# Performance work log

Measured on AMD Instinct MI355X. Metric: run time of the kernel, lower is better.

Reference implementation:

```python
import jax, jax.numpy as jnp
import numpy as np

INPUT_DIM = 1024
NUM_HEADS = 16
HEAD_DIM = INPUT_DIM // NUM_HEADS


def setup_inputs() -> dict:
    key = jax.random.key(0)
    ks = jax.random.split(key, 9)
    d = INPUT_DIM
    s = 1.0 / np.sqrt(d)
    x = jax.random.normal(ks[0], (2, 2048, d), dtype=jnp.float32)
    # nn.Linear default init ~ U(-1/sqrt(in), 1/sqrt(in)); weights stored as (out, in), we keep (in, out)
    Wq = jax.random.uniform(ks[1], (d, d), jnp.float32, -s, s)
    bq = jax.random.uniform(ks[2], (d,), jnp.float32, -s, s)
    Wk = jax.random.uniform(ks[3], (d, d), jnp.float32, -s, s)
    bk = jax.random.uniform(ks[4], (d,), jnp.float32, -s, s)
    Wv = jax.random.uniform(ks[5], (d, d), jnp.float32, -s, s)
    bv = jax.random.uniform(ks[6], (d,), jnp.float32, -s, s)
    Wo = jax.random.uniform(ks[7], (d, d), jnp.float32, -s, s)
    bo = jax.random.uniform(ks[8], (d,), jnp.float32, -s, s)
    return {"x": x, "Wq": Wq, "bq": bq, "Wk": Wk, "bk": bk, "Wv": Wv, "bv": bv, "Wo": Wo, "bo": bo}


def reference(x, Wq, bq, Wk, bk, Wv, bv, Wo, bo):
    b, t, d = x.shape
    h, hd = NUM_HEADS, HEAD_DIM
    # projections -> [b, h, t, hd]
    q = (x @ Wq + bq).reshape(b, t, h, hd).transpose(0, 2, 1, 3)
    k = (x @ Wk + bk).reshape(b, t, h, hd).transpose(0, 2, 1, 3)
    v = (x @ Wv + bv).reshape(b, t, h, hd).transpose(0, 2, 1, 3)
    scores = jnp.einsum('bhqd,bhkd->bhqk', q, k) / jnp.sqrt(jnp.float32(hd))
    probs = jax.nn.softmax(scores, axis=-1)
    out = jnp.einsum('bhqk,bhkd->bhqd', probs, v)
    out = out.transpose(0, 2, 1, 3).reshape(b, t, d)
    return out @ Wo + bo
```

## Files before the change

kernel.cpp:

```cpp
#include <hip/hip_runtime.h>
#include <math.h>


#define BATCH 2
#define SEQ   2048
#define DIM   1024
#define NHEAD 16
#define HDIM  64
#define MROWS (BATCH * SEQ)
#define BH    (BATCH * NHEAD)

typedef __attribute__((ext_vector_type(4))) float     floatx4;
typedef __attribute__((ext_vector_type(4))) float     float4v;
typedef __attribute__((ext_vector_type(8))) _Float16  half8;
typedef __attribute__((ext_vector_type(4))) _Float16  half4;
typedef __attribute__((ext_vector_type(2))) __fp16    fp16x2;

#define SOFT_C 5.77078016f
#define QSCALE 0.18033688f

#if __has_builtin(__builtin_amdgcn_exp2f)
#define EXP2F(x) __builtin_amdgcn_exp2f(x)
#else
#define EXP2F(x) exp2f(x)
#endif

__device__ __forceinline__ void gload16(const void* g, void* l) {
    __builtin_amdgcn_global_load_lds(
        (const __attribute__((address_space(1))) unsigned int*)g,
        (__attribute__((address_space(3))) unsigned int*)l, 16, 0, 0);
}

__device__ __forceinline__ unsigned pk2(float a, float b) {
    fp16x2 v = __builtin_amdgcn_cvt_pkrtz(a, b);
    return __builtin_bit_cast(unsigned, v);
}

__global__ __launch_bounds__(256) void prep(
    const float* __restrict__ x,
    const float* __restrict__ Wq, const float* __restrict__ Wk,
    const float* __restrict__ Wv, const float* __restrict__ Wo,
    _Float16* __restrict__ xh,
    _Float16* __restrict__ Wqt, _Float16* __restrict__ Wkt,
    _Float16* __restrict__ Wvt, _Float16* __restrict__ Wot)
{
    const int tid = threadIdx.x;
    if (blockIdx.z == 4) {
        const int bid = blockIdx.y * 16 + blockIdx.x;
        #pragma unroll
        for (int it = 0; it < 8; ++it) {
            const size_t i = (((size_t)it * 256 + bid) * 256 + tid) * 8;
            float4v a = *(const float4v*)(x + i);
            float4v b = *(const float4v*)(x + i + 4);
            half8 o;
            #pragma unroll
            for (int c = 0; c < 4; ++c) { o[c] = (_Float16)a[c]; o[4+c] = (_Float16)b[c]; }
            *(half8*)(xh + i) = o;
        }
        return;
    }
    __shared__ float tile[64][65];
    const float* W; _Float16* o;
    switch (blockIdx.z) {
        case 0: W = Wq; o = Wqt; break;
        case 1: W = Wk; o = Wkt; break;
        case 2: W = Wv; o = Wvt; break;
        default: W = Wo; o = Wot; break;
    }
    const int n0 = blockIdx.x * 64, k0 = blockIdx.y * 64;
    #pragma unroll
    for (int p = 0; p < 16; ++p) {
        int idx = tid + p * 256;
        int r = idx >> 6, c = idx & 63;
        tile[r][c] = W[(size_t)(k0 + r) * DIM + n0 + c];
    }
    __syncthreads();
    #pragma unroll
    for (int p = 0; p < 16; ++p) {
        int idx = tid + p * 256;
        int r = idx >> 6, c = idx & 63;
        o[(size_t)(n0 + r) * DIM + k0 + c] = (_Float16)tile[c][r];
    }
}

__device__ __forceinline__ void gemm_core16(
    const _Float16* __restrict__ Ap, const _Float16* __restrict__ Bp,
    int m0, int n0, _Float16* AL, _Float16* BL, floatx4 acc[4][4])
{
    const int tid  = threadIdx.x;
    const int wave = tid >> 6;
    const int lane = tid & 63;
    const int li   = lane & 15;
    const int quad = lane >> 4;
    const int wm   = (wave >> 1) * 64;
    const int wn   = (wave & 1) * 64;

    for (int kt = 0; kt < DIM / 64; ++kt) {
        __syncthreads();
        const int k0 = kt * 64;
        #pragma unroll
        for (int p = 0; p < 4; ++p) {
            int s = tid + p * 256;
            int r = s >> 3, ks = s & 7;
            int kg = (ks ^ (r & 7)) << 3;
            int ldsb = (wave * 64 + p * 256) * 8;
            gload16(Ap + (size_t)(m0 + r) * DIM + k0 + kg, AL + ldsb);
            gload16(Bp + (size_t)(n0 + r) * DIM + k0 + kg, BL + ldsb);
        }
        __syncthreads();

        half8 a[4][2], b[4][2];
        #pragma unroll
        for (int i = 0; i < 4; ++i) {
            int ra = (wm + i * 16 + li) << 6;
            int rb = (wn + i * 16 + li) << 6;
            #pragma unroll
            for (int h = 0; h < 2; ++h) {
                a[i][h] = *(const half8*)(AL + ra + (((h * 4 + quad) ^ (li & 7)) << 3));
                b[i][h] = *(const half8*)(BL + rb + (((h * 4 + quad) ^ (li & 7)) << 3));
            }
        }
        #pragma unroll
        for (int i = 0; i < 4; ++i)
            #pragma unroll
            for (int j = 0; j < 4; ++j) {
                acc[i][j] = __builtin_amdgcn_mfma_f32_16x16x32_f16(a[i][0], b[j][0], acc[i][j], 0, 0, 0);
                acc[i][j] = __builtin_amdgcn_mfma_f32_16x16x32_f16(a[i][1], b[j][1], acc[i][j], 0, 0, 0);
            }
    }
}

__global__ __launch_bounds__(256, 3) void qkv_mfma(
    const _Float16* __restrict__ xh,
    const _Float16* __restrict__ Wqt, const _Float16* __restrict__ Wkt,
    const _Float16* __restrict__ Wvt,
    const float* __restrict__ bq, const float* __restrict__ bk,
    const float* __restrict__ bv,
    _Float16* __restrict__ Qh, _Float16* __restrict__ Kh,
    _Float16* __restrict__ Vth)
{
    __shared__ __align__(16) _Float16 SH[128 * 136];
    _Float16* AL = SH;
    _Float16* BL = SH + 128 * 64;

    const int z = blockIdx.z;
    const _Float16* Bp; const float* bias;
    if (z == 0)      { Bp = Wqt; bias = bq; }
    else if (z == 1) { Bp = Wkt; bias = bk; }
    else             { Bp = Wvt; bias = bv; }

    const int m0 = blockIdx.y * 128, n0 = blockIdx.x * 128;

    floatx4 acc[4][4];
    #pragma unroll
    for (int i = 0; i < 4; ++i)
        #pragma unroll
        for (int j = 0; j < 4; ++j) acc[i][j] = (floatx4){0.f, 0.f, 0.f, 0.f};

    gemm_core16(xh, Bp, m0, n0, AL, BL, acc);

    const int tid = threadIdx.x, wave = tid >> 6, lane = tid & 63;
    const int li = lane & 15, quad = lane >> 4;
    const int wm = (wave >> 1) * 64, wn = (wave & 1) * 64;
    const int bb = m0 >> 11, t0 = m0 & 2047;

    if (z != 2) {
        _Float16* out = (z == 0) ? Qh : Kh;
        const float sc = (z == 0) ? QSCALE : 1.0f;
        #pragma unroll
        for (int i = 0; i < 4; ++i)
            #pragma unroll
            for (int j = 0; j < 4; ++j) {
                int n = n0 + wn + j * 16 + li;
                int h = n >> 6, hd = n & 63;
                float b_ = bias[n];
                #pragma unroll
                for (int r = 0; r < 4; ++r) {
                    int m = m0 + wm + i * 16 + quad * 4 + r;
                    int t = m & 2047;
                    out[(((size_t)(bb * NHEAD + h) * SEQ) + t) * HDIM + hd] =
                        (_Float16)((acc[i][j][r] + b_) * sc);
                }
            }
    } else {
        __syncthreads();
        #pragma unroll
        for (int i = 0; i < 4; ++i)
            #pragma unroll
            for (int j = 0; j < 4; ++j) {
                int n = wn + j * 16 + li;
                float b_ = bias[n0 + n];
                half4 w;
                #pragma unroll
                for (int r = 0; r < 4; ++r) w[r] = (_Float16)(acc[i][j][r] + b_);
                *(half4*)(SH + n * 136 + wm + i * 16 + quad * 4) = w;
            }
        __syncthreads();
        #pragma unroll
        for (int p = 0; p < 8; ++p) {
            int idx = p * 256 + tid;
            int v = idx >> 4, c8 = (idx & 15) * 8;
            half8 w = *(const half8*)(SH + v * 136 + c8);
            int n = n0 + v;
            int h = n >> 6, hd = n & 63;
            *(half8*)(Vth + ((size_t)(bb * NHEAD + h) * HDIM + hd) * SEQ + t0 + c8) = w;
        }
    }
}

#define LDP 72

__global__ __launch_bounds__(256) void attn(
    const _Float16* __restrict__ Q, const _Float16* __restrict__ K,
    const _Float16* __restrict__ Vt, _Float16* __restrict__ Ctx)
{
    __shared__ __align__(16) _Float16 Ks[64 * 64];
    __shared__ __align__(16) _Float16 Vs[64 * 64];
    __shared__ __align__(16) _Float16 Pt[4][32 * LDP];

    const int tid  = threadIdx.x;
    const int wave = tid >> 6;
    const int lane = tid & 63;
    const int li   = lane & 15;
    const int quad = lane >> 4;
    const int bh   = blockIdx.y;
    const int q0   = blockIdx.x * 128;
    const int b    = bh >> 4, h = bh & 15;

    half8 qa[2][2];
    #pragma unroll
    for (int nq = 0; nq < 2; ++nq) {
        size_t qrow = ((size_t)bh * SEQ + q0 + wave * 32 + nq * 16 + li) * HDIM;
        qa[nq][0] = *(const half8*)(Q + qrow + quad * 8);
        qa[nq][1] = *(const half8*)(Q + qrow + 32 + quad * 8);
    }

    half8 onesA;
    {
        _Float16 v = (li == 0) ? (_Float16)1.0f : (_Float16)0.0f;
        #pragma unroll
        for (int c = 0; c < 8; ++c) onesA[c] = v;
    }

    floatx4 O[4][2];
    floatx4 rsacc[2];
    #pragma unroll
    for (int nq = 0; nq < 2; ++nq) {
        rsacc[nq] = (floatx4){0.f, 0.f, 0.f, 0.f};
        #pragma unroll
        for (int i = 0; i < 4; ++i) O[i][nq] = (floatx4){0.f, 0.f, 0.f, 0.f};
    }

    const _Float16* Kbh = K  + (size_t)bh * SEQ * HDIM;
    const _Float16* Vbh = Vt + (size_t)bh * HDIM * SEQ;
    _Float16* Pw = Pt[wave];

    for (int kt = 0; kt < SEQ / 64; ++kt) {
        __syncthreads();
        {
            const _Float16* Kg = Kbh + (size_t)kt * 64 * HDIM;
            const _Float16* Vg = Vbh + kt * 64;
            #pragma unroll
            for (int p = 0; p < 2; ++p) {
                int s = tid + p * 256;
                int r = s >> 3, ks = s & 7;
                int kg = (ks ^ (r & 7)) << 3;
                int ldsb = (wave * 64 + p * 256) * 8;
                gload16(Kg + r * HDIM + kg, (_Float16*)Ks + ldsb);
                gload16(Vg + (size_t)r * SEQ + kg, (_Float16*)Vs + ldsb);
            }
        }
        __syncthreads();

        #pragma unroll
        for (int mb = 0; mb < 4; ++mb) {
            int row = (mb * 16 + li) << 6;
            half8 a0 = *(const half8*)(Ks + row + ((quad ^ (li & 7)) << 3));
            half8 a1 = *(const half8*)(Ks + row + (((quad + 4) ^ (li & 7)) << 3));
            #pragma unroll
            for (int nq = 0; nq < 2; ++nq) {
                floatx4 st = (floatx4){-SOFT_C, -SOFT_C, -SOFT_C, -SOFT_C};
                st = __builtin_amdgcn_mfma_f32_16x16x32_f16(a0, qa[nq][0], st, 0, 0, 0);
                st = __builtin_amdgcn_mfma_f32_16x16x32_f16(a1, qa[nq][1], st, 0, 0, 0);
                uint2 w;
                w.x = pk2(EXP2F(st[0]), EXP2F(st[1]));
                w.y = pk2(EXP2F(st[2]), EXP2F(st[3]));
                *(uint2*)(Pw + (nq * 16 + li) * LDP + mb * 16 + quad * 4) = w;
            }
        }

        half8 pb[2][2];
        #pragma unroll
        for (int nq = 0; nq < 2; ++nq) {
            pb[nq][0] = *(const half8*)(Pw + (nq * 16 + li) * LDP + quad * 8);
            pb[nq][1] = *(const half8*)(Pw + (nq * 16 + li) * LDP + 32 + quad * 8);
        }
        #pragma unroll
        for (int nq = 0; nq < 2; ++nq) {
            rsacc[nq] = __builtin_amdgcn_mfma_f32_16x16x32_f16(onesA, pb[nq][0], rsacc[nq], 0, 0, 0);
            rsacc[nq] = __builtin_amdgcn_mfma_f32_16x16x32_f16(onesA, pb[nq][1], rsacc[nq], 0, 0, 0);
        }
        #pragma unroll
        for (int mb = 0; mb < 4; ++mb) {
            int row = (mb * 16 + li) << 6;
            half8 v0 = *(const half8*)(Vs + row + ((quad ^ (li & 7)) << 3));
            half8 v1 = *(const half8*)(Vs + row + (((quad + 4) ^ (li & 7)) << 3));
            #pragma unroll
            for (int nq = 0; nq < 2; ++nq) {
                O[mb][nq] = __builtin_amdgcn_mfma_f32_16x16x32_f16(v0, pb[nq][0], O[mb][nq], 0, 0, 0);
                O[mb][nq] = __builtin_amdgcn_mfma_f32_16x16x32_f16(v1, pb[nq][1], O[mb][nq], 0, 0, 0);
            }
        }
    }

    float inv[2];
    #pragma unroll
    for (int nq = 0; nq < 2; ++nq) {
        float r = __shfl(rsacc[nq][0], li, 64);
        inv[nq] = 1.0f / r;
    }

    #pragma unroll
    for (int mb = 0; mb < 4; ++mb)
        #pragma unroll
        for (int nq = 0; nq < 2; ++nq) {
            uint2 w;
            w.x = pk2(O[mb][nq][0] * inv[nq], O[mb][nq][1] * inv[nq]);
            w.y = pk2(O[mb][nq][2] * inv[nq], O[mb][nq][3] * inv[nq]);
            *(uint2*)(Pw + (nq * 16 + li) * LDP + mb * 16 + quad * 4) = w;
        }
    #pragma unroll
    for (int p = 0; p < 4; ++p) {
        int idx = p * 64 + lane;
        int qq = idx >> 3, c8 = (idx & 7) * 8;
        half8 v = *(const half8*)(Pw + qq * LDP + c8);
        size_t row = (size_t)b * SEQ + q0 + wave * 32 + qq;
        *(half8*)(Ctx + row * DIM + h * HDIM + c8) = v;
    }
}

__global__ __launch_bounds__(256, 3) void out_mfma(
    const _Float16* __restrict__ Ctx, const _Float16* __restrict__ Wot,
    const float* __restrict__ bo, float* __restrict__ out)
{
    __shared__ __align__(16) _Float16 AL[128 * 64];
    __shared__ __align__(16) _Float16 BL[128 * 64];

    const int m0 = blockIdx.y * 128, n0 = blockIdx.x * 128;

    floatx4 acc[4][4];
    #pragma unroll
    for (int i = 0; i < 4; ++i)
        #pragma unroll
        for (int j = 0; j < 4; ++j) acc[i][j] = (floatx4){0.f, 0.f, 0.f, 0.f};

    gemm_core16(Ctx, Wot, m0, n0, AL, BL, acc);

    const int tid = threadIdx.x, wave = tid >> 6, lane = tid & 63;
    const int li = lane & 15, quad = lane >> 4;
    const int wm = (wave >> 1) * 64, wn = (wave & 1) * 64;

    #pragma unroll
    for (int i = 0; i < 4; ++i)
        #pragma unroll
        for (int j = 0; j < 4; ++j) {
            int n = n0 + wn + j * 16 + li;
            float b_ = bo[n];
            #pragma unroll
            for (int r = 0; r < 4; ++r) {
                int m = m0 + wm + i * 16 + quad * 4 + r;
                out[(size_t)m * DIM + n] = acc[i][j][r] + b_;
            }
        }
}

extern "C" void kernel_launch(void* const* d_in, const int* in_sizes, int n_in,
                              void* d_out, int out_size, void* d_ws, size_t ws_size,
                              hipStream_t stream) {
    const float* x  = (const float*)d_in[0];
    const float* Wq = (const float*)d_in[1];
    const float* bq = (const float*)d_in[2];
    const float* Wk = (const float*)d_in[3];
    const float* bk = (const float*)d_in[4];
    const float* Wv = (const float*)d_in[5];
    const float* bv = (const float*)d_in[6];
    const float* Wo = (const float*)d_in[7];
    const float* bo = (const float*)d_in[8];
    float* out = (float*)d_out;

    const size_t PX = (size_t)MROWS * DIM;
    const size_t PW = (size_t)DIM * DIM;
    _Float16* xh  = (_Float16*)d_ws;
    _Float16* Wqt = xh + PX;
    _Float16* Wkt = Wqt + PW;
    _Float16* Wvt = Wkt + PW;
    _Float16* Wot = Wvt + PW;
    _Float16* Qh  = Wot + PW;
    _Float16* Kh  = Qh + PX;
    _Float16* Vth = Kh + PX;

    _Float16* Ctx = xh;

    prep<<<dim3(16, 16, 5), 256, 0, stream>>>(
        x, Wq, Wk, Wv, Wo, xh, Wqt, Wkt, Wvt, Wot);

    qkv_mfma<<<dim3(DIM / 128, MROWS / 128, 3), 256, 0, stream>>>(
        xh, Wqt, Wkt, Wvt, bq, bk, bv, Qh, Kh, Vth);

    attn<<<dim3(SEQ / 128, BH), 256, 0, stream>>>(Qh, Kh, Vth, Ctx);

    out_mfma<<<dim3(DIM / 128, MROWS / 128), 256, 0, stream>>>(
        Ctx, Wot, bo, out);
}
```

Baseline: 201.2 us.

## Double-buffer K/V tiles in attention and relax GEMM launch bounds

The attention kernel now keeps two LDS buffers for the K and V tiles. It issues the global-to-LDS loads for the next key tile before computing on the current one, which hides load latency and removes one barrier per iteration. The cost is twice the LDS for K/V, which may lower attention occupancy. The QKV and output GEMM kernels also drop the minimum blocks-per-CU hint from 3 to 2, giving the compiler more register room at the cost of possible occupancy.

```diff
diff --git a/kernel.cpp b/kernel.cpp
--- a/kernel.cpp
+++ b/kernel.cpp
@@ -130,7 +130,7 @@
     }
 }
 
-__global__ __launch_bounds__(256, 3) void qkv_mfma(
+__global__ __launch_bounds__(256, 2) void qkv_mfma(
     const _Float16* __restrict__ xh,
     const _Float16* __restrict__ Wqt, const _Float16* __restrict__ Wkt,
     const _Float16* __restrict__ Wvt,
@@ -214,8 +214,8 @@
     const _Float16* __restrict__ Q, const _Float16* __restrict__ K,
     const _Float16* __restrict__ Vt, _Float16* __restrict__ Ctx)
 {
-    __shared__ __align__(16) _Float16 Ks[64 * 64];
-    __shared__ __align__(16) _Float16 Vs[64 * 64];
+    __shared__ __align__(16) _Float16 Ks[2][64 * 64];
+    __shared__ __align__(16) _Float16 Vs[2][64 * 64];
     __shared__ __align__(16) _Float16 Pt[4][32 * LDP];
 
     const int tid  = threadIdx.x;
@@ -255,28 +255,38 @@
     const _Float16* Vbh = Vt + (size_t)bh * HDIM * SEQ;
     _Float16* Pw = Pt[wave];
 
+    const int s0r = tid >> 3,           s0k = tid & 7;
+    const int s1r = (tid + 256) >> 3,   s1k = (tid + 256) & 7;
+    const int kg0 = (s0k ^ (s0r & 7)) << 3;
+    const int kg1 = (s1k ^ (s1r & 7)) << 3;
+    const int lb0 = (wave * 64) * 8;
+    const int lb1 = (wave * 64 + 256) * 8;
+
+    #define STAGE(buf, kt)                                                     \
+        do {                                                                   \
+            const _Float16* Kg = Kbh + (size_t)(kt) * 64 * HDIM;               \
+            const _Float16* Vg = Vbh + (kt) * 64;                              \
+            gload16(Kg + s0r * HDIM + kg0, Ks[buf] + lb0);                     \
+            gload16(Vg + (size_t)s0r * SEQ + kg0, Vs[buf] + lb0);              \
+            gload16(Kg + s1r * HDIM + kg1, Ks[buf] + lb1);                     \
+            gload16(Vg + (size_t)s1r * SEQ + kg1, Vs[buf] + lb1);              \
+        } while (0)
+
+    STAGE(0, 0);
+
     for (int kt = 0; kt < SEQ / 64; ++kt) {
+        const int cur = kt & 1;
         __syncthreads();
-        {
-            const _Float16* Kg = Kbh + (size_t)kt * 64 * HDIM;
-            const _Float16* Vg = Vbh + kt * 64;
-            #pragma unroll
-            for (int p = 0; p < 2; ++p) {
-                int s = tid + p * 256;
-                int r = s >> 3, ks = s & 7;
-                int kg = (ks ^ (r & 7)) << 3;
-                int ldsb = (wave * 64 + p * 256) * 8;
-                gload16(Kg + r * HDIM + kg, (_Float16*)Ks + ldsb);
-                gload16(Vg + (size_t)r * SEQ + kg, (_Float16*)Vs + ldsb);
-            }
-        }
-        __syncthreads();
+        if (kt + 1 < SEQ / 64) STAGE(cur ^ 1, kt + 1);
+
+        const _Float16* Kc = Ks[cur];
+        const _Float16* Vc = Vs[cur];
 
         #pragma unroll
         for (int mb = 0; mb < 4; ++mb) {
             int row = (mb * 16 + li) << 6;
-            half8 a0 = *(const half8*)(Ks + row + ((quad ^ (li & 7)) << 3));
-            half8 a1 = *(const half8*)(Ks + row + (((quad + 4) ^ (li & 7)) << 3));
+            half8 a0 = *(const half8*)(Kc + row + ((quad ^ (li & 7)) << 3));
+            half8 a1 = *(const half8*)(Kc + row + (((quad + 4) ^ (li & 7)) << 3));
             #pragma unroll
             for (int nq = 0; nq < 2; ++nq) {
                 floatx4 st = (floatx4){-SOFT_C, -SOFT_C, -SOFT_C, -SOFT_C};
@@ -303,8 +313,8 @@
         #pragma unroll
         for (int mb = 0; mb < 4; ++mb) {
             int row = (mb * 16 + li) << 6;
-            half8 v0 = *(const half8*)(Vs + row + ((quad ^ (li & 7)) << 3));
-            half8 v1 = *(const half8*)(Vs + row + (((quad + 4) ^ (li & 7)) << 3));
+            half8 v0 = *(const half8*)(Vc + row + ((quad ^ (li & 7)) << 3));
+            half8 v1 = *(const half8*)(Vc + row + (((quad + 4) ^ (li & 7)) << 3));
             #pragma unroll
             for (int nq = 0; nq < 2; ++nq) {
                 O[mb][nq] = __builtin_amdgcn_mfma_f32_16x16x32_f16(v0, pb[nq][0], O[mb][nq], 0, 0, 0);
@@ -312,6 +322,7 @@
             }
         }
     }
+    #undef STAGE
 
     float inv[2];
     #pragma unroll
@@ -339,7 +350,7 @@
     }
 }
 
-__global__ __launch_bounds__(256, 3) void out_mfma(
+__global__ __launch_bounds__(256, 2) void out_mfma(
     const _Float16* __restrict__ Ctx, const _Float16* __restrict__ Wot,
     const float* __restrict__ bo, float* __restrict__ out)
 {
```

Result: slower. 206.0 us (+2.4%).

## Load K/V fragments directly from global into registers with double buffering

Applied to the files above, without the earlier changes.

Drops the shared-memory staging of K and V tiles and the two block barriers per tile in the attention kernel. Each wave now loads its own K and V MFMA fragments straight from global memory into registers, double-buffered so the next tile's loads overlap the current tile's math. Because the tile is no longer shared, each of the four waves fetches the same K/V data separately, which quadruples global/L2 traffic and raises register pressure. The launch-bounds occupancy hints on all three kernels are also lowered from 3 to 2 to leave room for the extra registers.

```diff
diff --git a/kernel.cpp b/kernel.cpp
--- a/kernel.cpp
+++ b/kernel.cpp
@@ -130,7 +130,7 @@
     }
 }
 
-__global__ __launch_bounds__(256, 3) void qkv_mfma(
+__global__ __launch_bounds__(256, 2) void qkv_mfma(
     const _Float16* __restrict__ xh,
     const _Float16* __restrict__ Wqt, const _Float16* __restrict__ Wkt,
     const _Float16* __restrict__ Wvt,
@@ -210,12 +210,22 @@
 
 #define LDP 72
 
-__global__ __launch_bounds__(256) void attn(
+__device__ __forceinline__ void load_frag(
+    const _Float16* __restrict__ base, size_t rstride, int li, int quad,
+    half8 f[4][2])
+{
+    #pragma unroll
+    for (int mb = 0; mb < 4; ++mb) {
+        const _Float16* p = base + (size_t)(mb * 16 + li) * rstride + quad * 8;
+        f[mb][0] = *(const half8*)(p);
+        f[mb][1] = *(const half8*)(p + 32);
+    }
+}
+
+__global__ __launch_bounds__(256, 2) void attn(
     const _Float16* __restrict__ Q, const _Float16* __restrict__ K,
     const _Float16* __restrict__ Vt, _Float16* __restrict__ Ctx)
 {
-    __shared__ __align__(16) _Float16 Ks[64 * 64];
-    __shared__ __align__(16) _Float16 Vs[64 * 64];
     __shared__ __align__(16) _Float16 Pt[4][32 * LDP];
 
     const int tid  = threadIdx.x;
@@ -255,63 +265,58 @@
     const _Float16* Vbh = Vt + (size_t)bh * HDIM * SEQ;
     _Float16* Pw = Pt[wave];
 
-    for (int kt = 0; kt < SEQ / 64; ++kt) {
-        __syncthreads();
-        {
-            const _Float16* Kg = Kbh + (size_t)kt * 64 * HDIM;
-            const _Float16* Vg = Vbh + kt * 64;
-            #pragma unroll
-            for (int p = 0; p < 2; ++p) {
-                int s = tid + p * 256;
-                int r = s >> 3, ks = s & 7;
-                int kg = (ks ^ (r & 7)) << 3;
-                int ldsb = (wave * 64 + p * 256) * 8;
-                gload16(Kg + r * HDIM + kg, (_Float16*)Ks + ldsb);
-                gload16(Vg + (size_t)r * SEQ + kg, (_Float16*)Vs + ldsb);
-            }
-        }
-        __syncthreads();
-
-        #pragma unroll
-        for (int mb = 0; mb < 4; ++mb) {
-            int row = (mb * 16 + li) << 6;
-            half8 a0 = *(const half8*)(Ks + row + ((quad ^ (li & 7)) << 3));
-            half8 a1 = *(const half8*)(Ks + row + (((quad + 4) ^ (li & 7)) << 3));
-            #pragma unroll
-            for (int nq = 0; nq < 2; ++nq) {
-                floatx4 st = (floatx4){-SOFT_C, -SOFT_C, -SOFT_C, -SOFT_C};
-                st = __builtin_amdgcn_mfma_f32_16x16x32_f16(a0, qa[nq][0], st, 0, 0, 0);
-                st = __builtin_amdgcn_mfma_f32_16x16x32_f16(a1, qa[nq][1], st, 0, 0, 0);
-                uint2 w;
-                w.x = pk2(EXP2F(st[0]), EXP2F(st[1]));
-                w.y = pk2(EXP2F(st[2]), EXP2F(st[3]));
-                *(uint2*)(Pw + (nq * 16 + li) * LDP + mb * 16 + quad * 4) = w;
-            }
-        }
-
-        half8 pb[2][2];
-        #pragma unroll
-        for (int nq = 0; nq < 2; ++nq) {
-            pb[nq][0] = *(const half8*)(Pw + (nq * 16 + li) * LDP + quad * 8);
-            pb[nq][1] = *(const half8*)(Pw + (nq * 16 + li) * LDP + 32 + quad * 8);
-        }
-        #pragma unroll
-        for (int nq = 0; nq < 2; ++nq) {
-            rsacc[nq] = __builtin_amdgcn_mfma_f32_16x16x32_f16(onesA, pb[nq][0], rsacc[nq], 0, 0, 0);
-            rsacc[nq] = __builtin_amdgcn_mfma_f32_16x16x32_f16(onesA, pb[nq][1], rsacc[nq], 0, 0, 0);
-        }
-        #pragma unroll
-        for (int mb = 0; mb < 4; ++mb) {
-            int row = (mb * 16 + li) << 6;
-            half8 v0 = *(const half8*)(Vs + row + ((quad ^ (li & 7)) << 3));
-            half8 v1 = *(const half8*)(Vs + row + (((quad + 4) ^ (li & 7)) << 3));
-            #pragma unroll
-            for (int nq = 0; nq < 2; ++nq) {
-                O[mb][nq] = __builtin_amdgcn_mfma_f32_16x16x32_f16(v0, pb[nq][0], O[mb][nq], 0, 0, 0);
-                O[mb][nq] = __builtin_amdgcn_mfma_f32_16x16x32_f16(v1, pb[nq][1], O[mb][nq], 0, 0, 0);
-            }
-        }
-    }
+    #define ATTN_BODY(kf, vf)                                                  \
+        do {                                                                   \
+            _Pragma("unroll")                                                  \
+            for (int mb = 0; mb < 4; ++mb) {                                   \
+                _Pragma("unroll")                                              \
+                for (int nq = 0; nq < 2; ++nq) {                               \
+                    floatx4 st = (floatx4){-SOFT_C, -SOFT_C, -SOFT_C, -SOFT_C};\
+                    st = __builtin_amdgcn_mfma_f32_16x16x32_f16(kf[mb][0], qa[nq][0], st, 0, 0, 0); \
+                    st = __builtin_amdgcn_mfma_f32_16x16x32_f16(kf[mb][1], qa[nq][1], st, 0, 0, 0); \
+                    uint2 w;                                                   \
+                    w.x = pk2(EXP2F(st[0]), EXP2F(st[1]));                     \
+                    w.y = pk2(EXP2F(st[2]), EXP2F(st[3]));                     \
+                    *(uint2*)(Pw + (nq * 16 + li) * LDP + mb * 16 + quad * 4) = w; \
+                }                                                              \
+            }                                                                  \
+            half8 pb[2][2];                                                    \
+            _Pragma("unroll")                                                  \
+            for (int nq = 0; nq < 2; ++nq) {                                   \
+                pb[nq][0] = *(const half8*)(Pw + (nq * 16 + li) * LDP + quad * 8);      \
+                pb[nq][1] = *(const half8*)(Pw + (nq * 16 + li) * LDP + 32 + quad * 8); \
+            }                                                                  \
+            _Pragma("unroll")                                                  \
+            for (int nq = 0; nq < 2; ++nq) {                                   \
+                rsacc[nq] = __builtin_amdgcn_mfma_f32_16x16x32_f16(onesA, pb[nq][0], rsacc[nq], 0, 0, 0); \
+                rsacc[nq] = __builtin_amdgcn_mfma_f32_16x16x32_f16(onesA, pb[nq][1], rsacc[nq], 0, 0, 0); \
+            }                                                                  \
+            _Pragma("unroll")                                                  \
+            for (int mb = 0; mb < 4; ++mb) {                                   \
+                _Pragma("unroll")                                              \
+                for (int nq = 0; nq < 2; ++nq) {                               \
+                    O[mb][nq] = __builtin_amdgcn_mfma_f32_16x16x32_f16(vf[mb][0], pb[nq][0], O[mb][nq], 0, 0, 0); \
+                    O[mb][nq] = __builtin_amdgcn_mfma_f32_16x16x32_f16(vf[mb][1], pb[nq][1], O[mb][nq], 0, 0, 0); \
+                }                                                              \
+            }                                                                  \
+        } while (0)
+
+    half8 ka[4][2], va[4][2], kb[4][2], vb[4][2];
+    load_frag(Kbh, HDIM, li, quad, ka);
+    load_frag(Vbh, SEQ, li, quad, va);
+
+    #pragma unroll 1
+    for (int kt2 = 0; kt2 < SEQ / 128; ++kt2) {
+        load_frag(Kbh + (size_t)(kt2 * 2 + 1) * 64 * HDIM, HDIM, li, quad, kb);
+        load_frag(Vbh + (kt2 * 2 + 1) * 64,               SEQ,  li, quad, vb);
+        ATTN_BODY(ka, va);
+        if (kt2 + 1 < SEQ / 128) {
+            load_frag(Kbh + (size_t)(kt2 * 2 + 2) * 64 * HDIM, HDIM, li, quad, ka);
+            load_frag(Vbh + (kt2 * 2 + 2) * 64,               SEQ,  li, quad, va);
+        }
+        ATTN_BODY(kb, vb);
+    }
+    #undef ATTN_BODY
 
     float inv[2];
     #pragma unroll
@@ -339,7 +344,7 @@
     }
 }
 
-__global__ __launch_bounds__(256, 3) void out_mfma(
+__global__ __launch_bounds__(256, 2) void out_mfma(
     const _Float16* __restrict__ Ctx, const _Float16* __restrict__ Wot,
     const float* __restrict__ bo, float* __restrict__ out)
 {
```

Result: slower. 258.5 us (+28.5%).
